# Kernel tuning notes

Hardware: AMD Instinct MI355X
Metric: run time of the kernel (lower is better)

## Reference

```python
import jax, jax.numpy as jnp
import numpy as np

WS = 7    # window size
SS = 3    # shift size
NH = 6    # num heads
EPS = 1e-5


def _ln(x, g, b):
    m = jnp.mean(x, -1, keepdims=True)
    v = jnp.mean((x - m) ** 2, -1, keepdims=True)
    return (x - m) * jax.lax.rsqrt(v + EPS) * g + b


def _win_part(x, ws):
    # (B, H, W, C) -> (B*nW, ws*ws, C)
    B, H, W, C = x.shape
    x = x.reshape(B, H // ws, ws, W // ws, ws, C).transpose(0, 1, 3, 2, 4, 5)
    return x.reshape(-1, ws * ws, C)


def _win_rev(w, ws, B, H, W):
    # (B*nW, ws*ws, C) -> (B, H, W, C)
    C = w.shape[-1]
    x = w.reshape(B, H // ws, W // ws, ws, ws, C).transpose(0, 1, 3, 2, 4, 5)
    return x.reshape(B, H, W, C)


def _forward(x, norm1_g, norm1_b, qkv_w, qkv_b, proj_w, proj_b, norm2_g, norm2_b,
             fc1_w, fc1_b, fc2_w, fc2_b, rel_table, mask_matrix, H, W, rel_index):
    B, L, C = x.shape
    hd = C // NH
    shortcut = x
    h = _ln(x, norm1_g, norm1_b).reshape(B, H, W, C)
    pad_r = (WS - W % WS) % WS
    pad_b = (WS - H % WS) % WS
    h = jnp.pad(h, ((0, 0), (0, pad_b), (0, pad_r), (0, 0)))
    Hp, Wp = H + pad_b, W + pad_r
    # cyclic shift (shift_size > 0 path)
    h = jnp.roll(h, (-SS, -SS), axis=(1, 2))
    xw = _win_part(h, WS)                                   # [Bw, N, C]
    Bw, N, _ = xw.shape
    qkv = (xw @ qkv_w + qkv_b).reshape(Bw, N, 3, NH, hd)
    q = qkv[:, :, 0].transpose(0, 2, 1, 3) * (hd ** -0.5)   # [Bw, NH, N, hd]
    k = qkv[:, :, 1].transpose(0, 2, 1, 3)
    v = qkv[:, :, 2].transpose(0, 2, 1, 3)
    attn = q @ k.transpose(0, 1, 3, 2)                      # [Bw, NH, N, N]
    bias = rel_table[rel_index.reshape(-1)].reshape(N, N, NH).transpose(2, 0, 1)
    attn = attn + bias[None]
    nW = mask_matrix.shape[0]
    attn = attn.reshape(Bw // nW, nW, NH, N, N) + mask_matrix[None, :, None]
    attn = jax.nn.softmax(attn.reshape(Bw, NH, N, N), axis=-1)
    o = (attn @ v).transpose(0, 2, 1, 3).reshape(Bw, N, C)
    o = o @ proj_w + proj_b
    h = _win_rev(o, WS, B, Hp, Wp)
    h = jnp.roll(h, (SS, SS), axis=(1, 2))[:, :H, :W, :].reshape(B, L, C)
    x = shortcut + h
    y = _ln(x, norm2_g, norm2_b)
    y = jax.nn.gelu(y @ fc1_w + fc1_b, approximate=False) @ fc2_w + fc2_b  # torch GELU = exact erf
    return x + y


def setup_inputs() -> dict:
    B, H, W, C, HID = 32, 56, 56, 192, 768
    ws, ss = WS, SS
    ks = jax.random.split(jax.random.key(0), 8)
    rn = lambda i, shp, s: jax.random.normal(ks[i], shp, jnp.float32) * s
    inp = {
        'x': rn(0, (B, H * W, C), 1.0),
        'norm1_g': jnp.ones((C,), jnp.float32), 'norm1_b': jnp.zeros((C,), jnp.float32),
        'qkv_w': rn(1, (C, 3 * C), 0.02), 'qkv_b': jnp.zeros((3 * C,), jnp.float32),
        'proj_w': rn(2, (C, C), 0.02), 'proj_b': jnp.zeros((C,), jnp.float32),
        'norm2_g': jnp.ones((C,), jnp.float32), 'norm2_b': jnp.zeros((C,), jnp.float32),
        'fc1_w': rn(3, (C, HID), 0.02), 'fc1_b': jnp.zeros((HID,), jnp.float32),
        'fc2_w': rn(4, (HID, C), 0.02), 'fc2_b': jnp.zeros((C,), jnp.float32),
        'rel_table': rn(5, ((2 * ws - 1) ** 2, NH), 0.02),
    }
    # relative position index (same construction as torch buffer)
    coords = np.stack(np.meshgrid(np.arange(ws), np.arange(ws), indexing='ij')).reshape(2, -1)
    rel = (coords[:, :, None] - coords[:, None, :]).transpose(1, 2, 0)
    rel[..., 0] += ws - 1
    rel[..., 1] += ws - 1
    rel[..., 0] *= 2 * ws - 1
    inp['rel_index'] = jnp.asarray(rel.sum(-1), jnp.int32)  # [49, 49]
    # shifted-window attention mask (standard Swin construction)
    img = np.zeros((1, H, W, 1), np.float32)
    cnt = 0
    for hs in (slice(0, -ws), slice(-ws, -ss), slice(-ss, None)):
        for wsl in (slice(0, -ws), slice(-ws, -ss), slice(-ss, None)):
            img[:, hs, wsl, :] = cnt
            cnt += 1
    mw = img.reshape(1, H // ws, ws, W // ws, ws, 1).transpose(0, 1, 3, 2, 4, 5).reshape(-1, ws * ws)
    diff = mw[:, None, :] - mw[:, :, None]
    inp['mask_matrix'] = jnp.asarray(np.where(diff != 0, -100.0, 0.0), jnp.float32)  # [64, 49, 49]
    inp['H'] = H
    inp['W'] = W
    return inp


def reference(x, norm1_g, norm1_b, qkv_w, qkv_b, proj_w, proj_b, norm2_g, norm2_b,
              fc1_w, fc1_b, fc2_w, fc2_b, rel_table, rel_index, mask_matrix, H, W):
    return _forward(x, norm1_g, norm1_b, qkv_w, qkv_b, proj_w, proj_b, norm2_g, norm2_b,
                    fc1_w, fc1_b, fc2_w, fc2_b, rel_table, mask_matrix, H, W, rel_index)
```

## Files before the change

kernel.cpp:

```cpp
#include <hip/hip_runtime.h>

typedef __bf16 bf8 __attribute__((ext_vector_type(8)));
typedef float f4 __attribute__((ext_vector_type(4)));

__device__ __forceinline__ float b2f(unsigned short u) {
  union { unsigned int i; float f; } c; c.i = ((unsigned int)u) << 16; return c.f;
}
__device__ __forceinline__ unsigned short f2b(float f) {
  union { float f; unsigned int i; } c; c.f = f;
  unsigned int i = c.i;
  return (unsigned short)((i + 0x7FFFu + ((i >> 16) & 1u)) >> 16);
}

__device__ __forceinline__ void gl_lds16(const unsigned short* g, unsigned short* l) {
  __builtin_amdgcn_global_load_lds((const __attribute__((address_space(1))) unsigned int*)g,
                                   (__attribute__((address_space(3))) unsigned int*)l,
                                   16, 0, 0);
}

__device__ __forceinline__ float gelu_fast(float v) {
  float w = v * v;
  float u = v * (-1.59576912f - 0.07135481f * w);
  return v / (1.0f + __expf(u));
}

__global__ void transpose_kernel(const float* __restrict__ in,
                                 unsigned short* __restrict__ out, int K, int N) {
  int idx = blockIdx.x * 256 + threadIdx.x;
  if (idx < K * N) {
    int n = idx / K, k = idx - n * K;
    out[idx] = f2b(in[k * N + n]);
  }
}

__global__ __launch_bounds__(256) void ln_kernel(const float* __restrict__ xin,
                                                 const float* __restrict__ g,
                                                 const float* __restrict__ bb,
                                                 unsigned short* __restrict__ out) {
  long token = (long)blockIdx.x * 4 + (threadIdx.x >> 6);
  int lane = threadIdx.x & 63;
  const float* row = xin + token * 192;
  float v[3] = {row[lane], row[lane + 64], row[lane + 128]};
  float s = v[0] + v[1] + v[2];
#pragma unroll
  for (int m = 1; m < 64; m <<= 1) s += __shfl_xor(s, m, 64);
  float mean = s * (1.0f / 192.0f);
  float d0 = v[0] - mean, d1 = v[1] - mean, d2 = v[2] - mean;
  float dd = d0 * d0 + d1 * d1 + d2 * d2;
#pragma unroll
  for (int m = 1; m < 64; m <<= 1) dd += __shfl_xor(dd, m, 64);
  float rstd = rsqrtf(dd * (1.0f / 192.0f) + 1e-5f);
  unsigned short* orow = out + token * 192;
#pragma unroll
  for (int i = 0; i < 3; i++) {
    int c = lane + i * 64;
    orow[c] = f2b((v[i] - mean) * rstd * g[c] + bb[c]);
  }
}

template <int EPI>
__global__ __launch_bounds__(256) void gemm_kernel(const unsigned short* __restrict__ A,
                                                   const unsigned short* __restrict__ Bt,
                                                   const float* __restrict__ bias,
                                                   const float* __restrict__ res,
                                                   void* __restrict__ out, int K, int N) {
  __shared__ __align__(16) unsigned short As[2][128 * 64];
  __shared__ __align__(16) unsigned short Bs[2][64 * 64];
  const int tid = threadIdx.x;
  const int wave = tid >> 6;
  const int lane = tid & 63;
  const int quad = lane >> 4;
  const int l16 = lane & 15;

  const int NX = gridDim.x;
  int lin = blockIdx.y * NX + blockIdx.x;
  const int T = NX * gridDim.y;
  if ((T & 7) == 0) {
    lin = (lin & 7) * (T >> 3) + (lin >> 3);
  }
  const int bx = lin % NX;
  const int by = lin / NX;
  const long m0 = (long)by * 128;
  const long n0 = (long)bx * 64;

  long a_src[4];
  int a_dstc[4];
#pragma unroll
  for (int j = 0; j < 4; ++j) {
    int L = (wave * 4 + j) * 64 + lane;
    int row = L >> 3, cs = L & 7;
    a_src[j] = (m0 + row) * (long)K + ((cs ^ (row & 7)) << 3);
    a_dstc[j] = (wave * 4 + j) * 512;
  }
  long b_src[2];
  int b_dstc[2];
#pragma unroll
  for (int j = 0; j < 2; ++j) {
    int L = (wave * 2 + j) * 64 + lane;
    int row = L >> 3, cs = L & 7;
    b_src[j] = (n0 + row) * (long)K + ((cs ^ (row & 7)) << 3);
    b_dstc[j] = (wave * 2 + j) * 512;
  }

  const int nT = K >> 6;
  f4 acc[2][4] = {};

#pragma unroll
  for (int j = 0; j < 4; ++j) gl_lds16(A + a_src[j], &As[0][a_dstc[j]]);
#pragma unroll
  for (int j = 0; j < 2; ++j) gl_lds16(Bt + b_src[j], &Bs[0][b_dstc[j]]);

  int cur = 0;
  for (int t = 0; t < nT; ++t) {
    if (t + 1 < nT) {
      const int k0 = (t + 1) << 6;
#pragma unroll
      for (int j = 0; j < 4; ++j) gl_lds16(A + a_src[j] + k0, &As[cur ^ 1][a_dstc[j]]);
#pragma unroll
      for (int j = 0; j < 2; ++j) gl_lds16(Bt + b_src[j] + k0, &Bs[cur ^ 1][b_dstc[j]]);
    }
    __syncthreads();
#pragma unroll
    for (int kk = 0; kk < 2; ++kk) {
      bf8 a[2], b[4];
#pragma unroll
      for (int mt = 0; mt < 2; ++mt) {
        int r = wave * 32 + mt * 16 + l16;
        int c = kk * 4 + quad;
        a[mt] = *(const bf8*)&As[cur][r * 64 + ((c ^ (r & 7)) << 3)];
      }
#pragma unroll
      for (int nt = 0; nt < 4; ++nt) {
        int r = nt * 16 + l16;
        int c = kk * 4 + quad;
        b[nt] = *(const bf8*)&Bs[cur][r * 64 + ((c ^ (r & 7)) << 3)];
      }
#pragma unroll
      for (int mt = 0; mt < 2; ++mt)
#pragma unroll
        for (int nt = 0; nt < 4; ++nt)
          acc[mt][nt] = __builtin_amdgcn_mfma_f32_16x16x32_bf16(a[mt], b[nt], acc[mt][nt], 0, 0, 0);
    }
    __syncthreads();
    cur ^= 1;
  }

#pragma unroll
  for (int nt = 0; nt < 4; ++nt) {
    long n = n0 + nt * 16 + l16;
    float bv = bias[n];
#pragma unroll
    for (int mt = 0; mt < 2; ++mt) {
#pragma unroll
      for (int r = 0; r < 4; ++r) {
        long m = m0 + wave * 32 + mt * 16 + quad * 4 + r;
        float v = acc[mt][nt][r] + bv;
        long idx = m * N + n;
        if (EPI == 0) {
          ((unsigned short*)out)[idx] = f2b(v);
        } else if (EPI == 1) {
          ((float*)out)[idx] = v + res[idx];
        } else if (EPI == 2) {
          ((unsigned short*)out)[idx] = f2b(gelu_fast(v));
        } else {
          ((float*)out)[idx] = v + res[idx];
        }
      }
    }
  }
}

__global__ __launch_bounds__(128) void attn_kernel(const unsigned short* __restrict__ qkv,
                                                   const float* __restrict__ rel_t,
                                                   unsigned short* __restrict__ o) {
  __shared__ __align__(16) unsigned short sh[2 * 12032];
  __shared__ float relh[2][170];
  __shared__ int toksh[2][49];
  __shared__ int zsh[2][49];
  const int wave = threadIdx.x >> 6;
  const int lane = threadIdx.x & 63;
  const int quad = lane >> 4;
  const int l16 = lane & 15;
  const int p = blockIdx.x * 2 + wave;
  const int head = p % 6;
  const int wib = p / 6;
  const int wi = wib & 63;
  const int b = wib >> 6;
  unsigned short* Qs = sh + wave * 12032;
  unsigned short* Ks = Qs + 2560;
  unsigned short* Vts = Qs + 5120;
  unsigned short* Ps = Qs + 7424;

  if (lane < 49) {
    int r = lane / 7, c = lane - (lane / 7) * 7;
    int ph = (wi >> 3) * 7 + r, pw = (wi & 7) * 7 + c;
    int h = ph + 3; if (h >= 56) h -= 56;
    int w = pw + 3; if (w >= 56) w -= 56;
    toksh[wave][lane] = (b * 56 + h) * 56 + w;
    int zh = (ph < 49) ? 0 : (ph < 53 ? 1 : 2);
    int zw = (pw < 49) ? 0 : (pw < 53 ? 1 : 2);
    zsh[wave][lane] = zh * 3 + zw;
  }
  for (int i = lane; i < 169; i += 64) relh[wave][i] = rel_t[i * 6 + head];
  {
    unsigned int* qz = (unsigned int*)(Qs + 49 * 40);
    unsigned int* kz = (unsigned int*)(Ks + 49 * 40);
    for (int i = lane; i < 300; i += 64) { qz[i] = 0u; kz[i] = 0u; }
#pragma unroll
    for (int e = 0; e < 4; e++) {
      int ee = lane + e * 64;
      int d = ee >> 3, c8 = ee & 7;
      *(unsigned int*)&Vts[d * 72 + 48 + c8 * 2] = 0u;
    }
  }
  __syncthreads();

  for (int e = lane; e < 196; e += 64) {
    int n = e >> 2, c = e & 3;
    int t = toksh[wave][n];
    const uint4* src = (const uint4*)(qkv + (long)t * 576 + head * 32);
    uint4 qc = src[c];
    uint4 kc = src[c + 24];
    uint4 vc = src[c + 48];
    *(uint4*)&Qs[n * 40 + c * 8] = qc;
    *(uint4*)&Ks[n * 40 + c * 8] = kc;
    const unsigned short* vv = (const unsigned short*)&vc;
#pragma unroll
    for (int j = 0; j < 8; j++) Vts[(c * 8 + j) * 72 + n] = vv[j];
  }
  __syncthreads();

  bf8 af[4], bf_[4];
#pragma unroll
  for (int i = 0; i < 4; i++) af[i] = *(const bf8*)&Qs[(16 * i + l16) * 40 + quad * 8];
#pragma unroll
  for (int j = 0; j < 4; j++) bf_[j] = *(const bf8*)&Ks[(16 * j + l16) * 40 + quad * 8];
  f4 S[4][4];
#pragma unroll
  for (int i = 0; i < 4; i++)
#pragma unroll
    for (int j = 0; j < 4; j++)
      S[i][j] = __builtin_amdgcn_mfma_f32_16x16x32_bf16(af[i], bf_[j], (f4){0.f, 0.f, 0.f, 0.f}, 0, 0, 0);

  int colv[4], colkey[4], zcol[4];
#pragma unroll
  for (int jt = 0; jt < 4; jt++) {
    int col = 16 * jt + l16;
    int cc = col < 49 ? col : 48;
    int rj = cc / 7, cj = cc - rj * 7;
    colkey[jt] = rj * 13 + cj;
    zcol[jt] = zsh[wave][cc];
    colv[jt] = (col < 49);
  }

  const float sc = 0.17677669529663687f;
#pragma unroll
  for (int it = 0; it < 4; it++) {
#pragma unroll
    for (int r = 0; r < 4; r++) {
      int row = 16 * it + quad * 4 + r;
      int row2 = row < 49 ? row : 48;
      int ri = row2 / 7, ci = row2 - ri * 7;
      int rk = ri * 13 + ci + 84;
      int zr = zsh[wave][row2];
      float v[4];
#pragma unroll
      for (int jt = 0; jt < 4; jt++) {
        float bias = relh[wave][rk - colkey[jt]];
        float msk = (zr == zcol[jt]) ? 0.0f : -100.0f;
        float val = S[it][jt][r] * sc + bias + msk;
        v[jt] = colv[jt] ? val : -1e30f;
      }
      float mx = fmaxf(fmaxf(v[0], v[1]), fmaxf(v[2], v[3]));
#pragma unroll
      for (int m = 1; m < 16; m <<= 1) mx = fmaxf(mx, __shfl_xor(mx, m, 64));
      float e0 = __expf(v[0] - mx), e1 = __expf(v[1] - mx), e2 = __expf(v[2] - mx), e3 = __expf(v[3] - mx);
      float sum = e0 + e1 + e2 + e3;
#pragma unroll
      for (int m = 1; m < 16; m <<= 1) sum += __shfl_xor(sum, m, 64);
      float inv = 1.0f / sum;
      Ps[row * 72 + 0 + l16] = f2b(e0 * inv);
      Ps[row * 72 + 16 + l16] = f2b(e1 * inv);
      Ps[row * 72 + 32 + l16] = f2b(e2 * inv);
      Ps[row * 72 + 48 + l16] = f2b(e3 * inv);
    }
  }
  __syncthreads();

  f4 O[4][2] = {};
#pragma unroll
  for (int ks = 0; ks < 2; ks++) {
    bf8 pv[2];
#pragma unroll
    for (int nt = 0; nt < 2; nt++) pv[nt] = *(const bf8*)&Vts[(16 * nt + l16) * 72 + ks * 32 + quad * 8];
#pragma unroll
    for (int mt = 0; mt < 4; mt++) {
      bf8 pa = *(const bf8*)&Ps[(16 * mt + l16) * 72 + ks * 32 + quad * 8];
#pragma unroll
      for (int nt = 0; nt < 2; nt++)
        O[mt][nt] = __builtin_amdgcn_mfma_f32_16x16x32_bf16(pa, pv[nt], O[mt][nt], 0, 0, 0);
    }
  }
#pragma unroll
  for (int mt = 0; mt < 4; mt++) {
#pragma unroll
    for (int r = 0; r < 4; r++) {
      int row = 16 * mt + quad * 4 + r;
      if (row < 49) {
        long base = (long)toksh[wave][row] * 192 + head * 32 + l16;
        o[base] = f2b(O[mt][0][r]);
        o[base + 16] = f2b(O[mt][1][r]);
      }
    }
  }
}

extern "C" void kernel_launch(void* const* d_in, const int* in_sizes, int n_in,
                              void* d_out, int out_size, void* d_ws, size_t ws_size,
                              hipStream_t stream) {
  const float* x      = (const float*)d_in[0];
  const float* n1g    = (const float*)d_in[1];
  const float* n1b    = (const float*)d_in[2];
  const float* qkv_w  = (const float*)d_in[3];
  const float* qkv_b  = (const float*)d_in[4];
  const float* proj_w = (const float*)d_in[5];
  const float* proj_b = (const float*)d_in[6];
  const float* n2g    = (const float*)d_in[7];
  const float* n2b    = (const float*)d_in[8];
  const float* fc1_w  = (const float*)d_in[9];
  const float* fc1_b  = (const float*)d_in[10];
  const float* fc2_w  = (const float*)d_in[11];
  const float* fc2_b  = (const float*)d_in[12];
  const float* rel_t  = (const float*)d_in[13];
  const float* mask   = (const float*)d_in[15];
  (void)mask;

  char* ws = (char*)d_ws;
  unsigned short* qkv_wT  = (unsigned short*)(ws + 0);
  unsigned short* proj_wT = (unsigned short*)(ws + 221184);
  unsigned short* fc1_wT  = (unsigned short*)(ws + 294912);
  unsigned short* fc2_wT  = (unsigned short*)(ws + 589824);
  unsigned short* bufA    = (unsigned short*)(ws + 884736);
  unsigned short* bufB    = (unsigned short*)(ws + 39419904ULL);
  float*          xres    = (float*)(ws + 193560576ULL);

  const int M = 100352;

  transpose_kernel<<<(192 * 576 + 255) / 256, 256, 0, stream>>>(qkv_w, qkv_wT, 192, 576);
  transpose_kernel<<<(192 * 192 + 255) / 256, 256, 0, stream>>>(proj_w, proj_wT, 192, 192);
  transpose_kernel<<<(192 * 768 + 255) / 256, 256, 0, stream>>>(fc1_w, fc1_wT, 192, 768);
  transpose_kernel<<<(768 * 192 + 255) / 256, 256, 0, stream>>>(fc2_w, fc2_wT, 768, 192);

  ln_kernel<<<M / 4, 256, 0, stream>>>(x, n1g, n1b, bufA);
  gemm_kernel<0><<<dim3(576 / 64, M / 128), 256, 0, stream>>>(bufA, qkv_wT, qkv_b, nullptr, bufB, 192, 576);
  attn_kernel<<<12288 / 2, 128, 0, stream>>>(bufB, rel_t, bufA);
  gemm_kernel<1><<<dim3(192 / 64, M / 128), 256, 0, stream>>>(bufA, proj_wT, proj_b, x, xres, 192, 192);
  ln_kernel<<<M / 4, 256, 0, stream>>>(xres, n2g, n2b, bufA);
  gemm_kernel<2><<<dim3(768 / 64, M / 128), 256, 0, stream>>>(bufA, fc1_wT, fc1_b, nullptr, bufB, 192, 768);
  gemm_kernel<3><<<dim3(192 / 64, M / 128), 256, 0, stream>>>(bufB, fc2_wT, fc2_b, xres, d_out, 768, 192);
}
```

Measured before the change: 523.5 us.

## Load Q/K fragments directly from global and relax GEMM loop barriers

The attention kernel now loads the Q and K MFMA operands straight from global memory into registers instead of staging them through shared memory. This drops the Q/K LDS buffers, their zero-fill and one block barrier, and shrinks LDS use per block, which may allow more blocks per CU. Separately, the GEMM main loop replaces __syncthreads with explicit vmcnt waits plus raw s_barrier and sched_barrier, so the prefetch of the next tile can stay in flight. This relies on the hand-chosen wait count matching the number of outstanding loads.

```diff
diff --git a/kernel.cpp b/kernel.cpp
--- a/kernel.cpp
+++ b/kernel.cpp
@@ -118,8 +118,12 @@
       for (int j = 0; j < 4; ++j) gl_lds16(A + a_src[j] + k0, &As[cur ^ 1][a_dstc[j]]);
 #pragma unroll
       for (int j = 0; j < 2; ++j) gl_lds16(Bt + b_src[j] + k0, &Bs[cur ^ 1][b_dstc[j]]);
-    }
-    __syncthreads();
+      asm volatile("s_waitcnt vmcnt(6)" ::: "memory");
+    } else {
+      asm volatile("s_waitcnt vmcnt(0)" ::: "memory");
+    }
+    __builtin_amdgcn_s_barrier();
+    __builtin_amdgcn_sched_barrier(0);
 #pragma unroll
     for (int kk = 0; kk < 2; ++kk) {
       bf8 a[2], b[4];
@@ -141,7 +145,8 @@
         for (int nt = 0; nt < 4; ++nt)
           acc[mt][nt] = __builtin_amdgcn_mfma_f32_16x16x32_bf16(a[mt], b[nt], acc[mt][nt], 0, 0, 0);
     }
-    __syncthreads();
+    __builtin_amdgcn_sched_barrier(0);
+    __builtin_amdgcn_s_barrier();
     cur ^= 1;
   }
 
@@ -173,7 +178,7 @@
 __global__ __launch_bounds__(128) void attn_kernel(const unsigned short* __restrict__ qkv,
                                                    const float* __restrict__ rel_t,
                                                    unsigned short* __restrict__ o) {
-  __shared__ __align__(16) unsigned short sh[2 * 12032];
+  __shared__ __align__(16) unsigned short sh[2 * 6912];
   __shared__ float relh[2][170];
   __shared__ int toksh[2][49];
   __shared__ int zsh[2][49];
@@ -186,10 +191,8 @@
   const int wib = p / 6;
   const int wi = wib & 63;
   const int b = wib >> 6;
-  unsigned short* Qs = sh + wave * 12032;
-  unsigned short* Ks = Qs + 2560;
-  unsigned short* Vts = Qs + 5120;
-  unsigned short* Ps = Qs + 7424;
+  unsigned short* Vts = sh + wave * 6912;
+  unsigned short* Ps = Vts + 2304;
 
   if (lane < 49) {
     int r = lane / 7, c = lane - (lane / 7) * 7;
@@ -203,9 +206,6 @@
   }
   for (int i = lane; i < 169; i += 64) relh[wave][i] = rel_t[i * 6 + head];
   {
-    unsigned int* qz = (unsigned int*)(Qs + 49 * 40);
-    unsigned int* kz = (unsigned int*)(Ks + 49 * 40);
-    for (int i = lane; i < 300; i += 64) { qz[i] = 0u; kz[i] = 0u; }
 #pragma unroll
     for (int e = 0; e < 4; e++) {
       int ee = lane + e * 64;
@@ -218,23 +218,28 @@
   for (int e = lane; e < 196; e += 64) {
     int n = e >> 2, c = e & 3;
     int t = toksh[wave][n];
-    const uint4* src = (const uint4*)(qkv + (long)t * 576 + head * 32);
-    uint4 qc = src[c];
-    uint4 kc = src[c + 24];
-    uint4 vc = src[c + 48];
-    *(uint4*)&Qs[n * 40 + c * 8] = qc;
-    *(uint4*)&Ks[n * 40 + c * 8] = kc;
+    uint4 vc = *(const uint4*)(qkv + (long)t * 576 + head * 32 + 384 + c * 8);
     const unsigned short* vv = (const unsigned short*)&vc;
 #pragma unroll
     for (int j = 0; j < 8; j++) Vts[(c * 8 + j) * 72 + n] = vv[j];
   }
-  __syncthreads();
-
+
+  bf8 zv;
+#pragma unroll
+  for (int q8 = 0; q8 < 8; q8++) zv[q8] = (__bf16)0.0f;
   bf8 af[4], bf_[4];
 #pragma unroll
-  for (int i = 0; i < 4; i++) af[i] = *(const bf8*)&Qs[(16 * i + l16) * 40 + quad * 8];
-#pragma unroll
-  for (int j = 0; j < 4; j++) bf_[j] = *(const bf8*)&Ks[(16 * j + l16) * 40 + quad * 8];
+  for (int i = 0; i < 4; i++) {
+    int row = 16 * i + l16;
+    int rv = row < 49 ? row : 48;
+    long base = (long)toksh[wave][rv] * 576 + head * 32 + quad * 8;
+    bf8 qf = *(const bf8*)(qkv + base);
+    bf8 kf = *(const bf8*)(qkv + base + 192);
+    if (row >= 49) { qf = zv; kf = zv; }
+    af[i] = qf;
+    bf_[i] = kf;
+  }
+
   f4 S[4][4];
 #pragma unroll
   for (int i = 0; i < 4; i++)
@@ -252,6 +257,8 @@
     zcol[jt] = zsh[wave][cc];
     colv[jt] = (col < 49);
   }
+
+  __syncthreads();
 
   const float sc = 0.17677669529663687f;
 #pragma unroll
```

Result: faster. 506.4 us (-3.3%).
